# Optimization experiments

Measured on AMD Instinct MI355X. Metric: run time of the kernel, lower is better.

Reference implementation:

```python
import jax, jax.numpy as jnp
import numpy as np

N_NODES = 50000
N_EDGES = 800000
F_IN = 128
HID = 32
HEADS = 4
N_CLASSES = 16
N_GRAPHS = 64
EPS = 1e-5
NEG_SLOPE = 0.2


def setup_inputs() -> dict:
    key = jax.random.key(0)
    ks = jax.random.split(key, 12)
    x = jax.random.normal(ks[0], (N_NODES, F_IN), dtype=jnp.float32)
    edge_index = jax.random.randint(ks[1], (2, N_EDGES), 0, N_NODES, dtype=jnp.int64)
    batch = jnp.sort(jax.random.randint(ks[2], (N_NODES,), 0, N_GRAPHS, dtype=jnp.int64))
    # GATConv 1: F_IN -> HID per head, HEADS heads, concat
    W1 = jax.random.normal(ks[3], (F_IN, HEADS * HID), dtype=jnp.float32) / np.sqrt(F_IN)
    att_src1 = jax.random.normal(ks[4], (HEADS, HID), dtype=jnp.float32) / np.sqrt(HID)
    att_dst1 = jax.random.normal(ks[5], (HEADS, HID), dtype=jnp.float32) / np.sqrt(HID)
    bias1 = jnp.zeros((HEADS * HID,), dtype=jnp.float32)
    # GATConv 2: HEADS*HID -> N_CLASSES, 1 head, no concat
    W2 = jax.random.normal(ks[6], (HEADS * HID, N_CLASSES), dtype=jnp.float32) / np.sqrt(HEADS * HID)
    att_src2 = jax.random.normal(ks[7], (1, N_CLASSES), dtype=jnp.float32) / np.sqrt(N_CLASSES)
    att_dst2 = jax.random.normal(ks[8], (1, N_CLASSES), dtype=jnp.float32) / np.sqrt(N_CLASSES)
    bias2 = jnp.zeros((N_CLASSES,), dtype=jnp.float32)
    # BatchNorm affine params
    bn1_gamma = jnp.ones((F_IN,), dtype=jnp.float32)
    bn1_beta = jnp.zeros((F_IN,), dtype=jnp.float32)
    bn2_gamma = jnp.ones((HEADS * HID,), dtype=jnp.float32)
    bn2_beta = jnp.zeros((HEADS * HID,), dtype=jnp.float32)
    return dict(x=x, W1=W1, att_src1=att_src1, att_dst1=att_dst1, bias1=bias1,
                W2=W2, att_src2=att_src2, att_dst2=att_dst2, bias2=bias2,
                bn1_gamma=bn1_gamma, bn1_beta=bn1_beta,
                bn2_gamma=bn2_gamma, bn2_beta=bn2_beta,
                edge_index=edge_index, batch=batch)


def batchnorm(x, gamma, beta):
    mean = x.mean(axis=0)
    var = ((x - mean) ** 2).mean(axis=0)  # biased var, as torch BN uses for normalization
    return (x - mean) * jax.lax.rsqrt(var + EPS) * gamma + beta


def gat_conv(x, ei, W, a_src, a_dst, bias, heads, out_c, concat):
    N = x.shape[0]
    # add self loops (PyG default)
    loops = jnp.arange(N, dtype=ei.dtype)
    src = jnp.concatenate([ei[0], loops])
    dst = jnp.concatenate([ei[1], loops])
    h = (x @ W).reshape(N, heads, out_c)               # [N,H,C]
    a_s = (h * a_src).sum(-1)                          # [N,H]
    a_d = (h * a_dst).sum(-1)                          # [N,H]
    e = jax.nn.leaky_relu(a_s[src] + a_d[dst], NEG_SLOPE)  # [E,H]
    # softmax over incoming edges of each destination node
    emax = jax.ops.segment_max(e, dst, num_segments=N)[dst]
    ex = jnp.exp(e - emax)
    denom = jax.ops.segment_sum(ex, dst, num_segments=N)[dst]
    alpha = ex / denom                                  # [E,H]
    msg = h[src] * alpha[:, :, None]                    # [E,H,C]
    out = jax.ops.segment_sum(msg, dst, num_segments=N)  # [N,H,C]
    out = out.reshape(N, heads * out_c) if concat else out.mean(axis=1)
    return out + bias


def reference(x, W1, att_src1, att_dst1, bias1, W2, att_src2, att_dst2, bias2,
              bn1_gamma, bn1_beta, bn2_gamma, bn2_beta, edge_index, batch):
    h = batchnorm(x, bn1_gamma, bn1_beta)
    h = gat_conv(h, edge_index, W1, att_src1, att_dst1, bias1, HEADS, HID, True)
    h = jax.nn.relu(h)
    h = batchnorm(h, bn2_gamma, bn2_beta)
    h = gat_conv(h, edge_index, W2, att_src2, att_dst2, bias2, 1, N_CLASSES, False)
    h = jax.nn.gelu(h)
    # global mean pool over graphs
    sums = jax.ops.segment_sum(h, batch, num_segments=N_GRAPHS)
    counts = jax.ops.segment_sum(jnp.ones((h.shape[0],), h.dtype), batch, num_segments=N_GRAPHS)
    pooled = sums / jnp.maximum(counts, 1.0)[:, None]
    return jax.nn.log_softmax(pooled, axis=1)
```

## Files before the change

kernel.cpp:

```cpp
#include <hip/hip_runtime.h>
#include <math.h>
#include <stdint.h>

#define NN 50000
#define NE 800000
#define NG 64
#define NEG_SLOPE 0.2f
#define NBLK ((NN + 255) / 256)
#define BSH 8
#define NBUCK ((NN + 255) >> 8)

typedef unsigned short u16;
typedef __attribute__((ext_vector_type(8))) unsigned short ushort8;
typedef __attribute__((ext_vector_type(8))) short short8v;
typedef __attribute__((ext_vector_type(4))) float f32x4;

__device__ __forceinline__ float lrelu(float x) { return x > 0.f ? x : NEG_SLOPE * x; }
__device__ __forceinline__ float bf2f(u16 u) { return __uint_as_float(((unsigned)u) << 16); }
__device__ __forceinline__ u16 f2bf(float f) {
    unsigned b = __float_as_uint(f);
    return (u16)((b + 0x7FFF + ((b >> 16) & 1)) >> 16);
}

__global__ __launch_bounds__(256) void col_stats_kernel(const float* __restrict__ X, int nrows,
                                                        float* __restrict__ sum, float* __restrict__ ssum) {
    int tid = threadIdx.x;
    int c = tid & 127, half = tid >> 7;
    int rows_per = (nrows + gridDim.x - 1) / gridDim.x;
    int r0 = blockIdx.x * rows_per;
    int r1 = r0 + rows_per; if (r1 > nrows) r1 = nrows;
    float s = 0.f, ss = 0.f;
    for (int r = r0 + half; r < r1; r += 2) {
        float v = X[(size_t)r * 128 + c];
        s += v; ss += v * v;
    }
    __shared__ float sm1[256], sm2[256];
    sm1[tid] = s; sm2[tid] = ss;
    __syncthreads();
    if (tid < 128) {
        s = sm1[tid] + sm1[tid + 128];
        ss = sm2[tid] + sm2[tid + 128];
        atomicAdd(&sum[c], s);
        atomicAdd(&ssum[c], ss);
    }
}

__global__ __launch_bounds__(128) void bn_prep1_kernel(const float* __restrict__ sum, const float* __restrict__ ssum,
                                                       const float* __restrict__ gamma, const float* __restrict__ beta,
                                                       const float* __restrict__ W, float inv_n,
                                                       u16* __restrict__ WpT, float* __restrict__ hb) {
    int k = threadIdx.x;
    float mean = sum[k] * inv_n;
    float var = ssum[k] * inv_n - mean * mean;
    float a = gamma[k] * rsqrtf(var + 1e-5f);
    float b = beta[k] - mean * a;
    for (int j = 0; j < 128; j++) WpT[j * 128 + k] = f2bf(a * W[k * 128 + j]);
    __shared__ float bs[128];
    bs[k] = b;
    __syncthreads();
    float acc = 0.f;
    for (int kk = 0; kk < 128; kk++) acc += bs[kk] * W[kk * 128 + k];
    hb[k] = acc;
}

__global__ __launch_bounds__(128) void bn_prep_kernel(const float* __restrict__ sum, const float* __restrict__ ssum,
                                                      const float* __restrict__ gamma, const float* __restrict__ beta,
                                                      const float* __restrict__ W, int J, float inv_n,
                                                      float* __restrict__ Wp, float* __restrict__ hb) {
    int k = threadIdx.x;
    float mean = sum[k] * inv_n;
    float var = ssum[k] * inv_n - mean * mean;
    float a = gamma[k] * rsqrtf(var + 1e-5f);
    float b = beta[k] - mean * a;
    for (int j = 0; j < J; j++) Wp[k * J + j] = a * W[k * J + j];
    __shared__ float bs[128];
    bs[k] = b;
    __syncthreads();
    if (k < J) {
        float acc = 0.f;
        for (int kk = 0; kk < 128; kk++) acc += bs[kk] * W[kk * J + k];
        hb[k] = acc;
    }
}

__global__ __launch_bounds__(256) void gemm1_mfma_kernel(const float* __restrict__ X, const u16* __restrict__ WpT,
                                                         const float* __restrict__ hbias, const float* __restrict__ atts,
                                                         const float* __restrict__ attd, u16* __restrict__ Hb,
                                                         float* __restrict__ as_o, float* __restrict__ ad_o) {
    __shared__ u16 wlds[128][136];
    int tid = threadIdx.x;
    for (int u = tid; u < 2048; u += 256) {
        int c = u >> 4, ch = u & 15;
        *(ushort8*)&wlds[c][ch * 8] = *(const ushort8*)&WpT[c * 128 + ch * 8];
    }
    int lane = tid & 63;
    int wv = tid >> 6;
    int cl = lane & 15;
    int kg = lane >> 4;
    int row_base = blockIdx.x * 64 + wv * 16;
    int rr = min(row_base + cl, NN - 1);

    short8v afrag[4];
#pragma unroll
    for (int kb = 0; kb < 4; kb++) {
        const float* xp = &X[(size_t)rr * 128 + kb * 32 + kg * 8];
        float4 x0 = *(const float4*)xp;
        float4 x1 = *(const float4*)(xp + 4);
        ushort8 t;
        t[0] = f2bf(x0.x); t[1] = f2bf(x0.y); t[2] = f2bf(x0.z); t[3] = f2bf(x0.w);
        t[4] = f2bf(x1.x); t[5] = f2bf(x1.y); t[6] = f2bf(x1.z); t[7] = f2bf(x1.w);
        afrag[kb] = (short8v)t;
    }
    __syncthreads();

    f32x4 acc[8];
#pragma unroll
    for (int ct = 0; ct < 8; ct++) {
        f32x4 a = {0.f, 0.f, 0.f, 0.f};
#pragma unroll
        for (int kb = 0; kb < 4; kb++) {
            ushort8 bv = *(const ushort8*)&wlds[ct * 16 + cl][kb * 32 + kg * 8];
            a = __builtin_amdgcn_mfma_f32_16x16x32_bf16(afrag[kb], (short8v)bv, a, 0, 0, 0);
        }
        acc[ct] = a;
    }

#pragma unroll
    for (int reg = 0; reg < 4; reg++) {
        int r = row_base + kg * 4 + reg;
        bool valid = (r < NN);
        float sp[4] = {0.f, 0.f, 0.f, 0.f}, dp[4] = {0.f, 0.f, 0.f, 0.f};
#pragma unroll
        for (int ct = 0; ct < 8; ct++) {
            int c = ct * 16 + cl;
            float v = acc[ct][reg] + hbias[c];
            if (valid) Hb[(size_t)r * 128 + c] = f2bf(v);
            sp[ct >> 1] += v * atts[c];
            dp[ct >> 1] += v * attd[c];
        }
#pragma unroll
        for (int off = 1; off < 16; off <<= 1) {
#pragma unroll
            for (int h = 0; h < 4; h++) {
                sp[h] += __shfl_xor(sp[h], off);
                dp[h] += __shfl_xor(dp[h], off);
            }
        }
        if (valid) {
            if (cl < 4) as_o[r * 4 + cl] = sp[cl];
            else if (cl < 8) ad_o[r * 4 + (cl - 4)] = dp[cl - 4];
        }
    }
}

__global__ __launch_bounds__(256) void deg_hist_kernel(const int* __restrict__ dst, int* __restrict__ deg, int ne) {
    int e = blockIdx.x * 256 + threadIdx.x;
    if (e < ne) atomicAdd(&deg[dst[e]], 1);
}

__global__ __launch_bounds__(256) void scan_part_kernel(const int* __restrict__ deg, int* __restrict__ blocksum) {
    int i = blockIdx.x * 256 + threadIdx.x;
    int d = (i < NN) ? deg[i] : 0;
#pragma unroll
    for (int off = 1; off < 64; off <<= 1) d += __shfl_xor(d, off);
    __shared__ int sm[4];
    if ((threadIdx.x & 63) == 0) sm[threadIdx.x >> 6] = d;
    __syncthreads();
    if (threadIdx.x == 0) blocksum[blockIdx.x] = sm[0] + sm[1] + sm[2] + sm[3];
}

__global__ __launch_bounds__(256) void scan_block_kernel(const int* __restrict__ blocksum, int* __restrict__ blockoff) {
    __shared__ int sm[256];
    int tid = threadIdx.x;
    int v = (tid < NBLK) ? blocksum[tid] : 0;
    sm[tid] = v;
    __syncthreads();
    for (int off = 1; off < 256; off <<= 1) {
        int t = (tid >= off) ? sm[tid - off] : 0;
        __syncthreads();
        sm[tid] += t;
        __syncthreads();
    }
    if (tid < NBLK) blockoff[tid] = sm[tid] - v;
}

__global__ __launch_bounds__(256) void scan_final_kernel(const int* __restrict__ deg, const int* __restrict__ blockoff,
                                                         int* __restrict__ rowptr, int* __restrict__ bcur) {
    __shared__ int sm[256];
    int tid = threadIdx.x;
    int i = blockIdx.x * 256 + tid;
    int d = (i < NN) ? deg[i] : 0;
    sm[tid] = d;
    __syncthreads();
    for (int off = 1; off < 256; off <<= 1) {
        int t = (tid >= off) ? sm[tid - off] : 0;
        __syncthreads();
        sm[tid] += t;
        __syncthreads();
    }
    int excl = sm[tid] - d + blockoff[blockIdx.x];
    if (i < NN) {
        rowptr[i] = excl;
        if ((i & 255) == 0) bcur[i >> BSH] = excl;
    }
    if (i == NN - 1) rowptr[NN] = excl + d;
}

__global__ __launch_bounds__(256) void partition_kernel(const int* __restrict__ esrc, const int* __restrict__ edst,
                                                        int* __restrict__ bcur, int2* __restrict__ ebuf) {
    __shared__ int hist[NBUCK];
    __shared__ int cur[NBUCK];
    int tid = threadIdx.x;
    for (int b = tid; b < NBUCK; b += 256) hist[b] = 0;
    __syncthreads();
    int epb = (NE + gridDim.x - 1) / gridDim.x;
    int e0 = blockIdx.x * epb;
    int e1 = min(e0 + epb, NE);
    for (int e = e0 + tid; e < e1; e += 256)
        atomicAdd(&hist[edst[e] >> BSH], 1);
    __syncthreads();
    for (int b = tid; b < NBUCK; b += 256) {
        int h = hist[b];
        cur[b] = h ? atomicAdd(&bcur[b], h) : 0;
    }
    __syncthreads();
    for (int e = e0 + tid; e < e1; e += 256) {
        int s = esrc[e], d = edst[e];
        int pos = atomicAdd(&cur[d >> BSH], 1);
        ebuf[pos] = make_int2(s, d);
    }
}

__global__ __launch_bounds__(256) void fine_scatter_kernel(const int2* __restrict__ ebuf, const int* __restrict__ rowptr,
                                                           int* __restrict__ csr_src) {
    __shared__ int lcur[256];
    int b = blockIdx.x;
    int n0 = b << BSH;
    int n1 = min(n0 + 256, NN);
    int tid = threadIdx.x;
    if (n0 + tid < n1) lcur[tid] = rowptr[n0 + tid];
    __syncthreads();
    int e0 = rowptr[n0], e1 = rowptr[n1];
    for (int e = e0 + tid; e < e1; e += 256) {
        int2 p = ebuf[e];
        int pos = atomicAdd(&lcur[p.y - n0], 1);
        csr_src[pos] = p.x;
    }
}

__global__ __launch_bounds__(256) void gat1_agg_kernel(const u16* __restrict__ Hb, const float* __restrict__ as1,
                                                       const float* __restrict__ ad1, const int* __restrict__ rowptr,
                                                       const int* __restrict__ csr_src, const float* __restrict__ bias1,
                                                       float* __restrict__ out) {
    int n = blockIdx.x * 4 + (threadIdx.x >> 6);
    int lane = threadIdx.x & 63;
    int quarter = lane >> 4;
    int within = lane & 15;
    int head = within >> 2;
    int c8 = within * 8;
    int start = rowptr[n], end = rowptr[n + 1];

    float4 ad4 = *(const float4*)&ad1[n * 4];
    float4 as4 = *(const float4*)&as1[n * 4];
    float ps0 = __expf(lrelu(as4.x + ad4.x));
    float ps1 = __expf(lrelu(as4.y + ad4.y));
    float ps2 = __expf(lrelu(as4.z + ad4.z));
    float ps3 = __expf(lrelu(as4.w + ad4.w));
    float pselfh = (head == 0) ? ps0 : (head == 1) ? ps1 : (head == 2) ? ps2 : ps3;

    float acc[8];
    {
        ushort8 hv = *(const ushort8*)&Hb[(size_t)n * 128 + c8];
        float w = (quarter == 0) ? pselfh : 0.f;
#pragma unroll
        for (int k = 0; k < 8; k++) acc[k] = w * bf2f(hv[k]);
    }
    float d0 = 0.f, d1 = 0.f, d2 = 0.f, d3 = 0.f;

    for (int base = start; base < end; base += 64) {
        int i = base + lane;
        int s = 0;
        float p0 = 0.f, p1 = 0.f, p2 = 0.f, p3 = 0.f;
        if (i < end) {
            s = csr_src[i];
            float4 a = *(const float4*)&as1[(size_t)s * 4];
            p0 = __expf(lrelu(a.x + ad4.x));
            p1 = __expf(lrelu(a.y + ad4.y));
            p2 = __expf(lrelu(a.z + ad4.z));
            p3 = __expf(lrelu(a.w + ad4.w));
            d0 += p0; d1 += p1; d2 += p2; d3 += p3;
        }
        int cnt = min(64, end - base);
#pragma unroll 2
        for (int j = 0; j < cnt; j += 4) {
            int jj = j + quarter;
            int s0 = __shfl(s, jj);
            float q0 = __shfl(p0, jj);
            float q1 = __shfl(p1, jj);
            float q2 = __shfl(p2, jj);
            float q3 = __shfl(p3, jj);
            float pp = (head == 0) ? q0 : (head == 1) ? q1 : (head == 2) ? q2 : q3;
            if (jj < cnt) {
                ushort8 hv = *(const ushort8*)&Hb[(size_t)s0 * 128 + c8];
#pragma unroll
                for (int k = 0; k < 8; k++) acc[k] += pp * bf2f(hv[k]);
            }
        }
    }

#pragma unroll
    for (int off = 1; off < 64; off <<= 1) {
        d0 += __shfl_xor(d0, off);
        d1 += __shfl_xor(d1, off);
        d2 += __shfl_xor(d2, off);
        d3 += __shfl_xor(d3, off);
    }
    float den = ((head == 0) ? d0 : (head == 1) ? d1 : (head == 2) ? d2 : d3) + pselfh;
#pragma unroll
    for (int k = 0; k < 8; k++) {
        acc[k] += __shfl_xor(acc[k], 16);
        acc[k] += __shfl_xor(acc[k], 32);
    }
    if (quarter == 0) {
        float inv = 1.f / den;
        float4 b0 = *(const float4*)&bias1[c8];
        float4 b1 = *(const float4*)&bias1[c8 + 4];
        float4 o0, o1;
        o0.x = fmaxf(acc[0] * inv + b0.x, 0.f);
        o0.y = fmaxf(acc[1] * inv + b0.y, 0.f);
        o0.z = fmaxf(acc[2] * inv + b0.z, 0.f);
        o0.w = fmaxf(acc[3] * inv + b0.w, 0.f);
        o1.x = fmaxf(acc[4] * inv + b1.x, 0.f);
        o1.y = fmaxf(acc[5] * inv + b1.y, 0.f);
        o1.z = fmaxf(acc[6] * inv + b1.z, 0.f);
        o1.w = fmaxf(acc[7] * inv + b1.w, 0.f);
        *(float4*)&out[(size_t)n * 128 + c8] = o0;
        *(float4*)&out[(size_t)n * 128 + c8 + 4] = o1;
    }
}

__global__ __launch_bounds__(256) void gemm2_kernel(const float* __restrict__ X, const float* __restrict__ Wp,
                                                    const float* __restrict__ hb, const float* __restrict__ atts,
                                                    const float* __restrict__ attd, float* __restrict__ H2,
                                                    float* __restrict__ as_o, float* __restrict__ ad_o) {
    __shared__ float xs[16][129];
    __shared__ float wsm[128][16];
    __shared__ float hbs[16], ats[16], atd[16];
    int tid = threadIdx.x;
    if (tid < 16) { hbs[tid] = hb[tid]; ats[tid] = atts[tid]; atd[tid] = attd[tid]; }
    for (int u = tid; u < 2048; u += 256) wsm[u >> 4][u & 15] = Wp[u];
    int r0 = blockIdx.x * 16;
    for (int u = tid; u < 2048; u += 256) {
        int row = u >> 7, cc = u & 127;
        xs[row][cc] = X[(size_t)(r0 + row) * 128 + cc];
    }
    __syncthreads();
    int r = tid >> 4, c = tid & 15;
    float acc = 0.f;
#pragma unroll 8
    for (int k = 0; k < 128; k++) acc += xs[r][k] * wsm[k][c];
    acc += hbs[c];
    H2[(size_t)(r0 + r) * 16 + c] = acc;
    float s = acc * ats[c], d = acc * atd[c];
#pragma unroll
    for (int off = 1; off < 16; off <<= 1) {
        s += __shfl_xor(s, off);
        d += __shfl_xor(d, off);
    }
    if (c == 0) { as_o[r0 + r] = s; ad_o[r0 + r] = d; }
}

__global__ __launch_bounds__(256) void gat2_agg_kernel(const float* __restrict__ H2, const float* __restrict__ as2,
                                                       const float* __restrict__ ad2, const int* __restrict__ rowptr,
                                                       const int* __restrict__ csr_src, const float* __restrict__ bias2,
                                                       float* __restrict__ out) {
    int n = blockIdx.x * 4 + (threadIdx.x >> 6);
    int lane = threadIdx.x & 63;
    int quarter = lane >> 4;
    int c = lane & 15;
    int start = rowptr[n], end = rowptr[n + 1];
    float adn = ad2[n], asn = as2[n];
    float pself = __expf(lrelu(asn + adn));

    float acc = (quarter == 0) ? pself * H2[(size_t)n * 16 + c] : 0.f;
    float d = 0.f;

    for (int base = start; base < end; base += 64) {
        int i = base + lane;
        int s = 0;
        float p = 0.f;
        if (i < end) {
            s = csr_src[i];
            p = __expf(lrelu(as2[s] + adn));
            d += p;
        }
        int cnt = min(64, end - base);
#pragma unroll 2
        for (int j = 0; j < cnt; j += 4) {
            int jj = j + quarter;
            int s0 = __shfl(s, jj);
            float q = __shfl(p, jj);
            if (jj < cnt) acc += q * H2[(size_t)s0 * 16 + c];
        }
    }
#pragma unroll
    for (int off = 1; off < 64; off <<= 1) d += __shfl_xor(d, off);
    float den = d + pself;
    acc += __shfl_xor(acc, 16);
    acc += __shfl_xor(acc, 32);

    if (quarter == 0) {
        float xo = acc / den + bias2[c];
        float t = tanhf(0.7978845608028654f * (xo + 0.044715f * xo * xo * xo));
        out[(size_t)n * 16 + c] = 0.5f * xo * (1.f + t);
    }
}

__global__ __launch_bounds__(256) void pool_lsm_kernel(const float* __restrict__ X, const int* __restrict__ batch,
                                                       int nn, float* __restrict__ out) {
    int g = blockIdx.x;
    int tid = threadIdx.x;
    int lo = 0, hi = nn;
    while (lo < hi) { int mid = (lo + hi) >> 1; if (batch[mid] < g) lo = mid + 1; else hi = mid; }
    int s = lo;
    lo = s; hi = nn;
    while (lo < hi) { int mid = (lo + hi) >> 1; if (batch[mid] < g + 1) lo = mid + 1; else hi = mid; }
    int e2 = lo;
    int c = tid & 15, grp = tid >> 4;
    float acc = 0.f;
    for (int r = s + grp; r < e2; r += 16) acc += X[(size_t)r * 16 + c];
    __shared__ float sm[256];
    sm[tid] = acc;
    __syncthreads();
    for (int off = 8; off >= 1; off >>= 1) {
        if (grp < off) sm[tid] += sm[tid + off * 16];
        __syncthreads();
    }
    if (tid < 16) {
        float cnt = (float)(e2 - s);
        float v = sm[tid] / fmaxf(cnt, 1.f);
        float mx = v;
        mx = fmaxf(mx, __shfl_xor(mx, 1));
        mx = fmaxf(mx, __shfl_xor(mx, 2));
        mx = fmaxf(mx, __shfl_xor(mx, 4));
        mx = fmaxf(mx, __shfl_xor(mx, 8));
        float ex = __expf(v - mx);
        float ssum = ex;
        ssum += __shfl_xor(ssum, 1);
        ssum += __shfl_xor(ssum, 2);
        ssum += __shfl_xor(ssum, 4);
        ssum += __shfl_xor(ssum, 8);
        out[g * 16 + tid] = v - mx - __logf(ssum);
    }
}

extern "C" void kernel_launch(void* const* d_in, const int* in_sizes, int n_in,
                              void* d_out, int out_size, void* d_ws, size_t ws_size,
                              hipStream_t stream) {
    const float* x        = (const float*)d_in[0];
    const float* W1       = (const float*)d_in[1];
    const float* att_src1 = (const float*)d_in[2];
    const float* att_dst1 = (const float*)d_in[3];
    const float* bias1    = (const float*)d_in[4];
    const float* W2       = (const float*)d_in[5];
    const float* att_src2 = (const float*)d_in[6];
    const float* att_dst2 = (const float*)d_in[7];
    const float* bias2    = (const float*)d_in[8];
    const float* bn1g     = (const float*)d_in[9];
    const float* bn1b     = (const float*)d_in[10];
    const float* bn2g     = (const float*)d_in[11];
    const float* bn2b     = (const float*)d_in[12];
    const int*   ei       = (const int*)d_in[13];
    const int*   batch    = (const int*)d_in[14];
    float* out = (float*)d_out;

    char* p = (char*)d_ws;
    auto alloc = [&](size_t bytes) -> char* {
        char* r = p;
        p += (bytes + 255) & ~(size_t)255;
        return r;
    };
    float* bnbuf   = (float*)alloc(512 * sizeof(float));
    int*   deg     = (int*)alloc(NN * sizeof(int));
    int*   rowptr  = (int*)alloc((NN + 1) * sizeof(int));
    int*   bcur    = (int*)alloc(NBUCK * sizeof(int));
    int*   csr_src = (int*)alloc(NE * sizeof(int));
    int2*  ebuf    = (int2*)alloc((size_t)NE * sizeof(int2));
    int*   blocksum= (int*)alloc(NBLK * sizeof(int));
    int*   blockoff= (int*)alloc(NBLK * sizeof(int));
    u16*   W1pT    = (u16*)alloc(128 * 128 * sizeof(u16));
    float* h1bias  = (float*)alloc(128 * sizeof(float));
    u16*   h1b     = (u16*)alloc((size_t)NN * 128 * sizeof(u16));
    float* as1     = (float*)alloc((size_t)NN * 4 * sizeof(float));
    float* ad1     = (float*)alloc((size_t)NN * 4 * sizeof(float));
    float* out1    = (float*)alloc((size_t)NN * 128 * sizeof(float));
    float* W2p     = (float*)alloc(128 * 16 * sizeof(float));
    float* h2bias  = (float*)alloc(16 * sizeof(float));
    float* h2      = (float*)alloc((size_t)NN * 16 * sizeof(float));
    float* as2     = (float*)alloc(NN * sizeof(float));
    float* ad2     = (float*)alloc(NN * sizeof(float));
    float* out2g   = (float*)alloc((size_t)NN * 16 * sizeof(float));

    float* bn1sum = bnbuf;
    float* bn1ss  = bnbuf + 128;
    float* bn2sum = bnbuf + 256;
    float* bn2ss  = bnbuf + 384;
    const int* esrc = ei;
    const int* edst = ei + NE;

    hipMemsetAsync(bnbuf, 0, 512 * sizeof(float) + NN * sizeof(int), stream);

    const float inv_n = 1.f / (float)NN;

    col_stats_kernel<<<256, 256, 0, stream>>>(x, NN, bn1sum, bn1ss);
    bn_prep1_kernel<<<1, 128, 0, stream>>>(bn1sum, bn1ss, bn1g, bn1b, W1, inv_n, W1pT, h1bias);
    gemm1_mfma_kernel<<<(NN + 63) / 64, 256, 0, stream>>>(x, W1pT, h1bias, att_src1, att_dst1, h1b, as1, ad1);
    deg_hist_kernel<<<(NE + 255) / 256, 256, 0, stream>>>(edst, deg, NE);
    scan_part_kernel<<<NBLK, 256, 0, stream>>>(deg, blocksum);
    scan_block_kernel<<<1, 256, 0, stream>>>(blocksum, blockoff);
    scan_final_kernel<<<NBLK, 256, 0, stream>>>(deg, blockoff, rowptr, bcur);
    partition_kernel<<<256, 256, 0, stream>>>(esrc, edst, bcur, ebuf);
    fine_scatter_kernel<<<NBUCK, 256, 0, stream>>>(ebuf, rowptr, csr_src);
    gat1_agg_kernel<<<NN / 4, 256, 0, stream>>>(h1b, as1, ad1, rowptr, csr_src, bias1, out1);
    col_stats_kernel<<<256, 256, 0, stream>>>(out1, NN, bn2sum, bn2ss);
    bn_prep_kernel<<<1, 128, 0, stream>>>(bn2sum, bn2ss, bn2g, bn2b, W2, 16, inv_n, W2p, h2bias);
    gemm2_kernel<<<NN / 16, 256, 0, stream>>>(out1, W2p, h2bias, att_src2, att_dst2, h2, as2, ad2);
    gat2_agg_kernel<<<NN / 4, 256, 0, stream>>>(h2, as2, ad2, rowptr, csr_src, bias2, out2g);
    pool_lsm_kernel<<<NG, 256, 0, stream>>>(out2g, batch, NN, out);
}
```

Baseline: 351.9 us.

## Store layer-1 output in bf16, MFMA gemm2, and bucket-local CSR build

Replaces the per-node degree histogram and three-kernel scan with a per-bucket count, a single small scan, and per-bucket local degree counting and scanning inside fine_scatter. The layer-1 aggregation output is written as bf16 instead of fp32, which halves traffic for the BN2 stats pass and gemm2. gemm2 is rewritten to use bf16 MFMA with transposed scaled weights. This cuts kernel launches and global atomics but adds bf16 rounding of intermediate activations, which reduces accuracy.

```diff
diff --git a/kernel.cpp b/kernel.cpp
--- a/kernel.cpp
+++ b/kernel.cpp
@@ -6,7 +6,6 @@
 #define NE 800000
 #define NG 64
 #define NEG_SLOPE 0.2f
-#define NBLK ((NN + 255) / 256)
 #define BSH 8
 #define NBUCK ((NN + 255) >> 8)
 
@@ -32,6 +31,29 @@
     float s = 0.f, ss = 0.f;
     for (int r = r0 + half; r < r1; r += 2) {
         float v = X[(size_t)r * 128 + c];
+        s += v; ss += v * v;
+    }
+    __shared__ float sm1[256], sm2[256];
+    sm1[tid] = s; sm2[tid] = ss;
+    __syncthreads();
+    if (tid < 128) {
+        s = sm1[tid] + sm1[tid + 128];
+        ss = sm2[tid] + sm2[tid + 128];
+        atomicAdd(&sum[c], s);
+        atomicAdd(&ssum[c], ss);
+    }
+}
+
+__global__ __launch_bounds__(256) void col_stats_bf16_kernel(const u16* __restrict__ X, int nrows,
+                                                             float* __restrict__ sum, float* __restrict__ ssum) {
+    int tid = threadIdx.x;
+    int c = tid & 127, half = tid >> 7;
+    int rows_per = (nrows + gridDim.x - 1) / gridDim.x;
+    int r0 = blockIdx.x * rows_per;
+    int r1 = r0 + rows_per; if (r1 > nrows) r1 = nrows;
+    float s = 0.f, ss = 0.f;
+    for (int r = r0 + half; r < r1; r += 2) {
+        float v = bf2f(X[(size_t)r * 128 + c]);
         s += v; ss += v * v;
     }
     __shared__ float sm1[256], sm2[256];
@@ -63,22 +85,22 @@
     hb[k] = acc;
 }
 
-__global__ __launch_bounds__(128) void bn_prep_kernel(const float* __restrict__ sum, const float* __restrict__ ssum,
-                                                      const float* __restrict__ gamma, const float* __restrict__ beta,
-                                                      const float* __restrict__ W, int J, float inv_n,
-                                                      float* __restrict__ Wp, float* __restrict__ hb) {
+__global__ __launch_bounds__(128) void bn_prep2_kernel(const float* __restrict__ sum, const float* __restrict__ ssum,
+                                                       const float* __restrict__ gamma, const float* __restrict__ beta,
+                                                       const float* __restrict__ W, float inv_n,
+                                                       u16* __restrict__ WpT, float* __restrict__ hb) {
     int k = threadIdx.x;
     float mean = sum[k] * inv_n;
     float var = ssum[k] * inv_n - mean * mean;
     float a = gamma[k] * rsqrtf(var + 1e-5f);
     float b = beta[k] - mean * a;
-    for (int j = 0; j < J; j++) Wp[k * J + j] = a * W[k * J + j];
+    for (int j = 0; j < 16; j++) WpT[j * 128 + k] = f2bf(a * W[k * 16 + j]);
     __shared__ float bs[128];
     bs[k] = b;
     __syncthreads();
-    if (k < J) {
+    if (k < 16) {
         float acc = 0.f;
-        for (int kk = 0; kk < 128; kk++) acc += bs[kk] * W[kk * J + k];
+        for (int kk = 0; kk < 128; kk++) acc += bs[kk] * W[kk * 16 + k];
         hb[k] = acc;
     }
 }
@@ -153,26 +175,24 @@
     }
 }
 
-__global__ __launch_bounds__(256) void deg_hist_kernel(const int* __restrict__ dst, int* __restrict__ deg, int ne) {
-    int e = blockIdx.x * 256 + threadIdx.x;
-    if (e < ne) atomicAdd(&deg[dst[e]], 1);
-}
-
-__global__ __launch_bounds__(256) void scan_part_kernel(const int* __restrict__ deg, int* __restrict__ blocksum) {
-    int i = blockIdx.x * 256 + threadIdx.x;
-    int d = (i < NN) ? deg[i] : 0;
-#pragma unroll
-    for (int off = 1; off < 64; off <<= 1) d += __shfl_xor(d, off);
-    __shared__ int sm[4];
-    if ((threadIdx.x & 63) == 0) sm[threadIdx.x >> 6] = d;
-    __syncthreads();
-    if (threadIdx.x == 0) blocksum[blockIdx.x] = sm[0] + sm[1] + sm[2] + sm[3];
-}
-
-__global__ __launch_bounds__(256) void scan_block_kernel(const int* __restrict__ blocksum, int* __restrict__ blockoff) {
+__global__ __launch_bounds__(256) void bucket_count_kernel(const int* __restrict__ edst, int* __restrict__ bucket_cnt) {
+    __shared__ int hist[NBUCK];
+    int tid = threadIdx.x;
+    for (int b = tid; b < NBUCK; b += 256) hist[b] = 0;
+    __syncthreads();
+    int epb = (NE + gridDim.x - 1) / gridDim.x;
+    int e0 = blockIdx.x * epb;
+    int e1 = min(e0 + epb, NE);
+    for (int e = e0 + tid; e < e1; e += 256) atomicAdd(&hist[edst[e] >> BSH], 1);
+    __syncthreads();
+    for (int b = tid; b < NBUCK; b += 256) if (hist[b]) atomicAdd(&bucket_cnt[b], hist[b]);
+}
+
+__global__ __launch_bounds__(256) void scan196_kernel(const int* __restrict__ bucket_cnt,
+                                                      int* __restrict__ bucket_base, int* __restrict__ bcur) {
     __shared__ int sm[256];
     int tid = threadIdx.x;
-    int v = (tid < NBLK) ? blocksum[tid] : 0;
+    int v = (tid < NBUCK) ? bucket_cnt[tid] : 0;
     sm[tid] = v;
     __syncthreads();
     for (int off = 1; off < 256; off <<= 1) {
@@ -181,29 +201,12 @@
         sm[tid] += t;
         __syncthreads();
     }
-    if (tid < NBLK) blockoff[tid] = sm[tid] - v;
-}
-
-__global__ __launch_bounds__(256) void scan_final_kernel(const int* __restrict__ deg, const int* __restrict__ blockoff,
-                                                         int* __restrict__ rowptr, int* __restrict__ bcur) {
-    __shared__ int sm[256];
-    int tid = threadIdx.x;
-    int i = blockIdx.x * 256 + tid;
-    int d = (i < NN) ? deg[i] : 0;
-    sm[tid] = d;
-    __syncthreads();
-    for (int off = 1; off < 256; off <<= 1) {
-        int t = (tid >= off) ? sm[tid - off] : 0;
-        __syncthreads();
-        sm[tid] += t;
-        __syncthreads();
-    }
-    int excl = sm[tid] - d + blockoff[blockIdx.x];
-    if (i < NN) {
-        rowptr[i] = excl;
-        if ((i & 255) == 0) bcur[i >> BSH] = excl;
-    }
-    if (i == NN - 1) rowptr[NN] = excl + d;
+    if (tid < NBUCK) {
+        int ex = sm[tid] - v;
+        bucket_base[tid] = ex;
+        bcur[tid] = ex;
+    }
+    if (tid == NBUCK - 1) bucket_base[NBUCK] = sm[tid];
 }
 
 __global__ __launch_bounds__(256) void partition_kernel(const int* __restrict__ esrc, const int* __restrict__ edst,
@@ -231,16 +234,34 @@
     }
 }
 
-__global__ __launch_bounds__(256) void fine_scatter_kernel(const int2* __restrict__ ebuf, const int* __restrict__ rowptr,
-                                                           int* __restrict__ csr_src) {
+__global__ __launch_bounds__(256) void fine_scatter_kernel(const int2* __restrict__ ebuf,
+                                                           const int* __restrict__ bucket_base,
+                                                           int* __restrict__ rowptr, int* __restrict__ csr_src) {
+    __shared__ int ldeg[256];
+    __shared__ int ssc[256];
     __shared__ int lcur[256];
-    int b = blockIdx.x;
+    int b = blockIdx.x, tid = threadIdx.x;
     int n0 = b << BSH;
-    int n1 = min(n0 + 256, NN);
-    int tid = threadIdx.x;
-    if (n0 + tid < n1) lcur[tid] = rowptr[n0 + tid];
-    __syncthreads();
-    int e0 = rowptr[n0], e1 = rowptr[n1];
+    int e0 = bucket_base[b], e1 = bucket_base[b + 1];
+    ldeg[tid] = 0;
+    __syncthreads();
+    for (int e = e0 + tid; e < e1; e += 256) atomicAdd(&ldeg[ebuf[e].y - n0], 1);
+    __syncthreads();
+    int d = ldeg[tid];
+    ssc[tid] = d;
+    __syncthreads();
+    for (int off = 1; off < 256; off <<= 1) {
+        int t = (tid >= off) ? ssc[tid - off] : 0;
+        __syncthreads();
+        ssc[tid] += t;
+        __syncthreads();
+    }
+    int excl = e0 + ssc[tid] - d;
+    int n = n0 + tid;
+    if (n < NN) rowptr[n] = excl;
+    lcur[tid] = excl;
+    if (b == NBUCK - 1 && tid == 0) rowptr[NN] = e1;
+    __syncthreads();
     for (int e = e0 + tid; e < e1; e += 256) {
         int2 p = ebuf[e];
         int pos = atomicAdd(&lcur[p.y - n0], 1);
@@ -251,7 +272,7 @@
 __global__ __launch_bounds__(256) void gat1_agg_kernel(const u16* __restrict__ Hb, const float* __restrict__ as1,
                                                        const float* __restrict__ ad1, const int* __restrict__ rowptr,
                                                        const int* __restrict__ csr_src, const float* __restrict__ bias1,
-                                                       float* __restrict__ out) {
+                                                       u16* __restrict__ out) {
     int n = blockIdx.x * 4 + (threadIdx.x >> 6);
     int lane = threadIdx.x & 63;
     int quarter = lane >> 4;
@@ -325,49 +346,60 @@
         float inv = 1.f / den;
         float4 b0 = *(const float4*)&bias1[c8];
         float4 b1 = *(const float4*)&bias1[c8 + 4];
-        float4 o0, o1;
-        o0.x = fmaxf(acc[0] * inv + b0.x, 0.f);
-        o0.y = fmaxf(acc[1] * inv + b0.y, 0.f);
-        o0.z = fmaxf(acc[2] * inv + b0.z, 0.f);
-        o0.w = fmaxf(acc[3] * inv + b0.w, 0.f);
-        o1.x = fmaxf(acc[4] * inv + b1.x, 0.f);
-        o1.y = fmaxf(acc[5] * inv + b1.y, 0.f);
-        o1.z = fmaxf(acc[6] * inv + b1.z, 0.f);
-        o1.w = fmaxf(acc[7] * inv + b1.w, 0.f);
-        *(float4*)&out[(size_t)n * 128 + c8] = o0;
-        *(float4*)&out[(size_t)n * 128 + c8 + 4] = o1;
-    }
-}
-
-__global__ __launch_bounds__(256) void gemm2_kernel(const float* __restrict__ X, const float* __restrict__ Wp,
-                                                    const float* __restrict__ hb, const float* __restrict__ atts,
-                                                    const float* __restrict__ attd, float* __restrict__ H2,
-                                                    float* __restrict__ as_o, float* __restrict__ ad_o) {
-    __shared__ float xs[16][129];
-    __shared__ float wsm[128][16];
-    __shared__ float hbs[16], ats[16], atd[16];
-    int tid = threadIdx.x;
-    if (tid < 16) { hbs[tid] = hb[tid]; ats[tid] = atts[tid]; atd[tid] = attd[tid]; }
-    for (int u = tid; u < 2048; u += 256) wsm[u >> 4][u & 15] = Wp[u];
-    int r0 = blockIdx.x * 16;
-    for (int u = tid; u < 2048; u += 256) {
-        int row = u >> 7, cc = u & 127;
-        xs[row][cc] = X[(size_t)(r0 + row) * 128 + cc];
-    }
-    __syncthreads();
-    int r = tid >> 4, c = tid & 15;
-    float acc = 0.f;
-#pragma unroll 8
-    for (int k = 0; k < 128; k++) acc += xs[r][k] * wsm[k][c];
-    acc += hbs[c];
-    H2[(size_t)(r0 + r) * 16 + c] = acc;
-    float s = acc * ats[c], d = acc * atd[c];
-#pragma unroll
-    for (int off = 1; off < 16; off <<= 1) {
-        s += __shfl_xor(s, off);
-        d += __shfl_xor(d, off);
-    }
-    if (c == 0) { as_o[r0 + r] = s; ad_o[r0 + r] = d; }
+        ushort8 o;
+        o[0] = f2bf(fmaxf(acc[0] * inv + b0.x, 0.f));
+        o[1] = f2bf(fmaxf(acc[1] * inv + b0.y, 0.f));
+        o[2] = f2bf(fmaxf(acc[2] * inv + b0.z, 0.f));
+        o[3] = f2bf(fmaxf(acc[3] * inv + b0.w, 0.f));
+        o[4] = f2bf(fmaxf(acc[4] * inv + b1.x, 0.f));
+        o[5] = f2bf(fmaxf(acc[5] * inv + b1.y, 0.f));
+        o[6] = f2bf(fmaxf(acc[6] * inv + b1.z, 0.f));
+        o[7] = f2bf(fmaxf(acc[7] * inv + b1.w, 0.f));
+        *(ushort8*)&out[(size_t)n * 128 + c8] = o;
+    }
+}
+
+__global__ __launch_bounds__(256) void gemm2_mfma_kernel(const u16* __restrict__ Xb, const u16* __restrict__ W2pT,
+                                                         const float* __restrict__ hb, const float* __restrict__ atts,
+                                                         const float* __restrict__ attd, float* __restrict__ H2,
+                                                         float* __restrict__ as_o, float* __restrict__ ad_o) {
+    __shared__ u16 wlds[16][136];
+    int tid = threadIdx.x;
+    {
+        int c = tid >> 4, ch = tid & 15;
+        *(ushort8*)&wlds[c][ch * 8] = *(const ushort8*)&W2pT[c * 128 + ch * 8];
+    }
+    int lane = tid & 63, wv = tid >> 6;
+    int cl = lane & 15, kg = lane >> 4;
+    int row_base = blockIdx.x * 64 + wv * 16;
+    int rr = min(row_base + cl, NN - 1);
+    __syncthreads();
+
+    f32x4 a = {0.f, 0.f, 0.f, 0.f};
+#pragma unroll
+    for (int kb = 0; kb < 4; kb++) {
+        ushort8 av = *(const ushort8*)&Xb[(size_t)rr * 128 + kb * 32 + kg * 8];
+        ushort8 bv = *(const ushort8*)&wlds[cl][kb * 32 + kg * 8];
+        a = __builtin_amdgcn_mfma_f32_16x16x32_bf16((short8v)av, (short8v)bv, a, 0, 0, 0);
+    }
+    float ats = atts[cl], atd = attd[cl], hbc = hb[cl];
+#pragma unroll
+    for (int reg = 0; reg < 4; reg++) {
+        int r = row_base + kg * 4 + reg;
+        bool valid = (r < NN);
+        float v = a[reg] + hbc;
+        if (valid) H2[(size_t)r * 16 + cl] = v;
+        float s = v * ats, d = v * atd;
+#pragma unroll
+        for (int off = 1; off < 16; off <<= 1) {
+            s += __shfl_xor(s, off);
+            d += __shfl_xor(d, off);
+        }
+        if (valid) {
+            if (cl == 0) as_o[r] = s;
+            else if (cl == 1) ad_o[r] = d;
+        }
+    }
 }
 
 __global__ __launch_bounds__(256) void gat2_agg_kernel(const float* __restrict__ H2, const float* __restrict__ as2,
@@ -480,26 +512,25 @@
         p += (bytes + 255) & ~(size_t)255;
         return r;
     };
-    float* bnbuf   = (float*)alloc(512 * sizeof(float));
-    int*   deg     = (int*)alloc(NN * sizeof(int));
-    int*   rowptr  = (int*)alloc((NN + 1) * sizeof(int));
-    int*   bcur    = (int*)alloc(NBUCK * sizeof(int));
-    int*   csr_src = (int*)alloc(NE * sizeof(int));
-    int2*  ebuf    = (int2*)alloc((size_t)NE * sizeof(int2));
-    int*   blocksum= (int*)alloc(NBLK * sizeof(int));
-    int*   blockoff= (int*)alloc(NBLK * sizeof(int));
-    u16*   W1pT    = (u16*)alloc(128 * 128 * sizeof(u16));
-    float* h1bias  = (float*)alloc(128 * sizeof(float));
-    u16*   h1b     = (u16*)alloc((size_t)NN * 128 * sizeof(u16));
-    float* as1     = (float*)alloc((size_t)NN * 4 * sizeof(float));
-    float* ad1     = (float*)alloc((size_t)NN * 4 * sizeof(float));
-    float* out1    = (float*)alloc((size_t)NN * 128 * sizeof(float));
-    float* W2p     = (float*)alloc(128 * 16 * sizeof(float));
-    float* h2bias  = (float*)alloc(16 * sizeof(float));
-    float* h2      = (float*)alloc((size_t)NN * 16 * sizeof(float));
-    float* as2     = (float*)alloc(NN * sizeof(float));
-    float* ad2     = (float*)alloc(NN * sizeof(float));
-    float* out2g   = (float*)alloc((size_t)NN * 16 * sizeof(float));
+    float* bnbuf      = (float*)alloc(512 * sizeof(float));
+    int*   bucket_cnt = (int*)alloc(NBUCK * sizeof(int));
+    int*   bucket_base= (int*)alloc((NBUCK + 1) * sizeof(int));
+    int*   bcur       = (int*)alloc(NBUCK * sizeof(int));
+    int*   rowptr     = (int*)alloc((NN + 1) * sizeof(int));
+    int*   csr_src    = (int*)alloc(NE * sizeof(int));
+    int2*  ebuf       = (int2*)alloc((size_t)NE * sizeof(int2));
+    u16*   W1pT       = (u16*)alloc(128 * 128 * sizeof(u16));
+    float* h1bias     = (float*)alloc(128 * sizeof(float));
+    u16*   h1b        = (u16*)alloc((size_t)NN * 128 * sizeof(u16));
+    float* as1        = (float*)alloc((size_t)NN * 4 * sizeof(float));
+    float* ad1        = (float*)alloc((size_t)NN * 4 * sizeof(float));
+    u16*   out1b      = (u16*)alloc((size_t)NN * 128 * sizeof(u16));
+    u16*   W2pT       = (u16*)alloc(16 * 128 * sizeof(u16));
+    float* h2bias     = (float*)alloc(16 * sizeof(float));
+    float* h2         = (float*)alloc((size_t)NN * 16 * sizeof(float));
+    float* as2        = (float*)alloc(NN * sizeof(float));
+    float* ad2        = (float*)alloc(NN * sizeof(float));
+    float* out2g      = (float*)alloc((size_t)NN * 16 * sizeof(float));
 
     float* bn1sum = bnbuf;
     float* bn1ss  = bnbuf + 128;
@@ -508,23 +539,21 @@
     const int* esrc = ei;
     const int* edst = ei + NE;
 
-    hipMemsetAsync(bnbuf, 0, 512 * sizeof(float) + NN * sizeof(int), stream);
+    hipMemsetAsync(bnbuf, 0, 512 * sizeof(float) + NBUCK * sizeof(int), stream);
 
     const float inv_n = 1.f / (float)NN;
 
     col_stats_kernel<<<256, 256, 0, stream>>>(x, NN, bn1sum, bn1ss);
     bn_prep1_kernel<<<1, 128, 0, stream>>>(bn1sum, bn1ss, bn1g, bn1b, W1, inv_n, W1pT, h1bias);
     gemm1_mfma_kernel<<<(NN + 63) / 64, 256, 0, stream>>>(x, W1pT, h1bias, att_src1, att_dst1, h1b, as1, ad1);
-    deg_hist_kernel<<<(NE + 255) / 256, 256, 0, stream>>>(edst, deg, NE);
-    scan_part_kernel<<<NBLK, 256, 0, stream>>>(deg, blocksum);
-    scan_block_kernel<<<1, 256, 0, stream>>>(blocksum, blockoff);
-    scan_final_kernel<<<NBLK, 256, 0, stream>>>(deg, blockoff, rowptr, bcur);
+    bucket_count_kernel<<<256, 256, 0, stream>>>(edst, bucket_cnt);
+    scan196_kernel<<<1, 256, 0, stream>>>(bucket_cnt, bucket_base, bcur);
     partition_kernel<<<256, 256, 0, stream>>>(esrc, edst, bcur, ebuf);
-    fine_scatter_kernel<<<NBUCK, 256, 0, stream>>>(ebuf, rowptr, csr_src);
-    gat1_agg_kernel<<<NN / 4, 256, 0, stream>>>(h1b, as1, ad1, rowptr, csr_src, bias1, out1);
-    col_stats_kernel<<<256, 256, 0, stream>>>(out1, NN, bn2sum, bn2ss);
-    bn_prep_kernel<<<1, 128, 0, stream>>>(bn2sum, bn2ss, bn2g, bn2b, W2, 16, inv_n, W2p, h2bias);
-    gemm2_kernel<<<NN / 16, 256, 0, stream>>>(out1, W2p, h2bias, att_src2, att_dst2, h2, as2, ad2);
+    fine_scatter_kernel<<<NBUCK, 256, 0, stream>>>(ebuf, bucket_base, rowptr, csr_src);
+    gat1_agg_kernel<<<NN / 4, 256, 0, stream>>>(h1b, as1, ad1, rowptr, csr_src, bias1, out1b);
+    col_stats_bf16_kernel<<<256, 256, 0, stream>>>(out1b, NN, bn2sum, bn2ss);
+    bn_prep2_kernel<<<1, 128, 0, stream>>>(bn2sum, bn2ss, bn2g, bn2b, W2, inv_n, W2pT, h2bias);
+    gemm2_mfma_kernel<<<(NN + 63) / 64, 256, 0, stream>>>(out1b, W2pT, h2bias, att_src2, att_dst2, h2, as2, ad2);
     gat2_agg_kernel<<<NN / 4, 256, 0, stream>>>(h2, as2, ad2, rowptr, csr_src, bias2, out2g);
     pool_lsm_kernel<<<NG, 256, 0, stream>>>(out2g, batch, NN, out);
 }
```

Measured after the change: 308.4 us. 12.4% less time.
